# Optimization experiments

Measured on AMD Instinct MI355X. Metric: run time of the kernel, lower is better.

## Reference

```python
import jax, jax.numpy as jnp
import numpy as np

# Model hyperparameters (from init_kwargs)
CHANNEL_COUNT = 32   # C: features per element
MIXTURE_COUNT = 4    # K: number of class distributions
MIXTURE_SIZE = 4     # S: gaussian components per class
EM_ITERS = 3         # fixed EM refinement iterations
LOG2PI = 1.8378770664093453
COV_REG = 1e-4       # covariance diagonal regularizer
EPS = 1e-6


def setup_inputs() -> dict:
    key = jax.random.key(0)
    kf, kl = jax.random.split(key)
    features = jax.random.normal(kf, (4, CHANNEL_COUNT, 65536), dtype=jnp.float32)
    initial_labels = jax.random.randint(kl, (4, 65536), 0, MIXTURE_COUNT, dtype=jnp.int32)
    return {"features": features, "initial_labels": initial_labels}


def reference(features, initial_labels):
    # features: [B, C, N] float; initial_labels: [B, N] int in [0, K)
    B, C, N = features.shape
    K, S = MIXTURE_COUNT, MIXTURE_SIZE
    dt = features.dtype

    # class membership mask [B, K, N]
    mask = jax.nn.one_hot(initial_labels, K, dtype=dt).transpose(0, 2, 1)
    # deterministic initial within-class component assignment: element n -> component n % S
    comp_onehot = jax.nn.one_hot(jnp.arange(N) % S, S, dtype=dt).T  # [S, N]
    r = mask[:, :, None, :] * comp_onehot[None, None]               # [B, K, S, N]

    eye = COV_REG * jnp.eye(C, dtype=dt)
    logp = None
    for _ in range(EM_ITERS):
        # ---- M-step: per-component weight, mean, covariance (sufficient stats) ----
        w = r.sum(-1)                                                # [B, K, S]
        mu = jnp.einsum('bksn,bcn->bksc', r, features) / (w[..., None] + EPS)
        sxx = jnp.einsum('bksn,bcn,bdn->bkscd', r, features, features) / (w[..., None, None] + EPS)
        cov = sxx - jnp.einsum('bksc,bksd->bkscd', mu, mu) + eye     # [B, K, S, C, C]
        prec = jnp.linalg.inv(cov)
        _, logdet = jnp.linalg.slogdet(cov)                          # [B, K, S]
        pi = (w + EPS) / (w.sum(-1, keepdims=True) + S * EPS)        # mixing weights

        # ---- E-step: full-covariance gaussian log-density per element ----
        t = jnp.einsum('bkscd,bdn->bkscn', prec, features)           # [B, K, S, C, N]
        quad = (jnp.einsum('bcn,bkscn->bksn', features, t)
                - 2.0 * jnp.einsum('bksc,bkscn->bksn', mu, t)
                + jnp.einsum('bksc,bkscd,bksd->bks', mu, prec, mu)[..., None])
        logp = jnp.log(pi)[..., None] - 0.5 * (C * LOG2PI + logdet[..., None] + quad)  # [B,K,S,N]
        # responsibilities within each class, restricted to that class's labeled elements
        r = jax.nn.softmax(logp, axis=2) * mask[:, :, None, :]

    # per-class mixture log-likelihood for EVERY element, then posterior over classes
    class_ll = jax.nn.logsumexp(logp, axis=2)        # [B, K, N]
    output_logits = jax.nn.softmax(class_ll, axis=1)  # class assignment probabilities
    return output_logits
```

## Files before the change

### kernel.cpp

```cpp
#include <hip/hip_runtime.h>
#include <hip/hip_fp16.h>
#include <math.h>

#define BB 4
#define CC 32
#define KK 4
#define SS 4
#define NN 65536

constexpr int NCOMP = 64;
constexpr int SSTRIDE = 1088;
constexpr int PSTRIDE = 1128;
constexpr int NB = 128;
constexpr float EPS_ = 1e-6f;
constexpr float COVREG_ = 1e-4f;
constexpr float LOG2PI_C = 1.8378770664093453f;

__device__ constexpr int XOFF_[32] = {
    0,   4,   8,   12,  16,  24,  32,  40,  48,  60,  72,
    84,  96,  112, 128, 144, 160, 180, 200, 220, 240, 264,
    288, 312, 336, 364, 392, 420, 448, 480, 512, 544};

typedef _Float16 half8 __attribute__((ext_vector_type(8)));
typedef float floatx4 __attribute__((ext_vector_type(4)));

template <bool ITER0>
__global__ __launch_bounds__(256, 2) void gmm_accum_mfma(
    const float* __restrict__ feat, const int* __restrict__ labels,
    const float* __restrict__ resp, float* __restrict__ partials) {
  __shared__ __align__(16) float fC[32 * 36];
  __shared__ __align__(16) _Float16 respH[4][32];
  __shared__ __align__(16) _Float16 maskH[4][32];

  const int t = threadIdx.x;
  const int b = blockIdx.y;
  const int blk0 = blockIdx.x * 512;
  const int k = t >> 6;
  const int l = t & 63;
  const int row16 = l & 15;
  const int kg = l >> 4;

  floatx4 acc[4][7];
#pragma unroll
  for (int s = 0; s < 4; ++s)
#pragma unroll
    for (int j = 0; j < 7; ++j) acc[s][j] = (floatx4){0.f, 0.f, 0.f, 0.f};

  const int cstage = t >> 3;
  const int n4 = (t & 7) * 4;

  float4 pf;
  float4 presp = make_float4(0, 0, 0, 0);
  int plab = 0;
  pf = *(const float4*)(feat + ((size_t)b * CC + cstage) * NN + blk0 + n4);
  if (t < 32) {
    plab = labels[b * NN + blk0 + t];
    if (!ITER0) presp = *(const float4*)(resp + ((size_t)b * NN + blk0 + t) * 4);
  }

  const half8 hz = {0, 0, 0, 0, 0, 0, 0, 0};

  for (int chunk = 0; chunk < 16; ++chunk) {
    *(float4*)&fC[cstage * 36 + n4] = pf;
    if (t < 32) {
      if (ITER0) {
        const int cmp = (blk0 + chunk * 32 + t) & 3;
        respH[0][t] = (cmp == 0) ? (_Float16)1 : (_Float16)0;
        respH[1][t] = (cmp == 1) ? (_Float16)1 : (_Float16)0;
        respH[2][t] = (cmp == 2) ? (_Float16)1 : (_Float16)0;
        respH[3][t] = (cmp == 3) ? (_Float16)1 : (_Float16)0;
      } else {
        respH[0][t] = (_Float16)presp.x;
        respH[1][t] = (_Float16)presp.y;
        respH[2][t] = (_Float16)presp.z;
        respH[3][t] = (_Float16)presp.w;
      }
      maskH[0][t] = (plab == 0) ? (_Float16)1 : (_Float16)0;
      maskH[1][t] = (plab == 1) ? (_Float16)1 : (_Float16)0;
      maskH[2][t] = (plab == 2) ? (_Float16)1 : (_Float16)0;
      maskH[3][t] = (plab == 3) ? (_Float16)1 : (_Float16)0;
    }
    __syncthreads();

    if (chunk < 15) {
      const int n0n = blk0 + (chunk + 1) * 32;
      pf = *(const float4*)(feat + ((size_t)b * CC + cstage) * NN + n0n + n4);
      if (t < 32) {
        plab = labels[b * NN + n0n + t];
        if (!ITER0)
          presp = *(const float4*)(resp + ((size_t)b * NN + n0n + t) * 4);
      }
    }

    const float4 fa0 = *(const float4*)&fC[row16 * 36 + kg * 8];
    const float4 fa1 = *(const float4*)&fC[row16 * 36 + kg * 8 + 4];
    const float4 fb0 = *(const float4*)&fC[(row16 + 16) * 36 + kg * 8];
    const float4 fb1 = *(const float4*)&fC[(row16 + 16) * 36 + kg * 8 + 4];
    half8 ff0, ff1;
    ff0[0] = (_Float16)fa0.x; ff0[1] = (_Float16)fa0.y;
    ff0[2] = (_Float16)fa0.z; ff0[3] = (_Float16)fa0.w;
    ff0[4] = (_Float16)fa1.x; ff0[5] = (_Float16)fa1.y;
    ff0[6] = (_Float16)fa1.z; ff0[7] = (_Float16)fa1.w;
    ff1[0] = (_Float16)fb0.x; ff1[1] = (_Float16)fb0.y;
    ff1[2] = (_Float16)fb0.z; ff1[3] = (_Float16)fb0.w;
    ff1[4] = (_Float16)fb1.x; ff1[5] = (_Float16)fb1.y;
    ff1[6] = (_Float16)fb1.z; ff1[7] = (_Float16)fb1.w;

    const half8 mh = *(const half8*)&maskH[k][kg * 8];
    const half8 H0 = ff0 * mh;
    const half8 H1 = ff1 * mh;
    const half8 agB = (row16 == 0) ? mh : hz;

#pragma unroll
    for (int s = 0; s < 4; ++s) {
      const half8 rh = *(const half8*)&respH[s][kg * 8];
      const half8 G0 = ff0 * rh;
      const half8 G1 = ff1 * rh;
      const half8 agA = (row16 == 0) ? rh : hz;
      acc[s][0] =
          __builtin_amdgcn_mfma_f32_16x16x32_f16(G0, H0, acc[s][0], 0, 0, 0);
      acc[s][1] =
          __builtin_amdgcn_mfma_f32_16x16x32_f16(G0, H1, acc[s][1], 0, 0, 0);
      acc[s][2] =
          __builtin_amdgcn_mfma_f32_16x16x32_f16(G1, H0, acc[s][2], 0, 0, 0);
      acc[s][3] =
          __builtin_amdgcn_mfma_f32_16x16x32_f16(G1, H1, acc[s][3], 0, 0, 0);
      acc[s][4] =
          __builtin_amdgcn_mfma_f32_16x16x32_f16(G0, agB, acc[s][4], 0, 0, 0);
      acc[s][5] =
          __builtin_amdgcn_mfma_f32_16x16x32_f16(G1, agB, acc[s][5], 0, 0, 0);
      acc[s][6] =
          __builtin_amdgcn_mfma_f32_16x16x32_f16(agA, agB, acc[s][6], 0, 0, 0);
    }
    __syncthreads();
  }

#pragma unroll
  for (int s = 0; s < 4; ++s) {
    float* sg = partials +
                ((size_t)(b * NB + blockIdx.x) * 16 + (k * 4 + s)) * SSTRIDE;
    const int dr = kg * 4;
#pragma unroll
    for (int r = 0; r < 4; ++r) {
      sg[(dr + r) * 32 + row16] = acc[s][0][r];
      sg[(dr + r) * 32 + 16 + row16] = acc[s][1][r];
      sg[(16 + dr + r) * 32 + row16] = acc[s][2][r];
      sg[(16 + dr + r) * 32 + 16 + row16] = acc[s][3][r];
    }
    if (row16 == 0) {
#pragma unroll
      for (int r = 0; r < 4; ++r) {
        sg[1024 + dr + r] = acc[s][4][r];
        sg[1024 + 16 + dr + r] = acc[s][5][r];
      }
    }
    if (l == 0) sg[1056] = acc[s][6][0];
  }
}

template <bool ITER0, bool ATOMIC, int TILES>
__global__ __launch_bounds__(256, 1) void gmm_accum(
    const float* __restrict__ feat, const int* __restrict__ labels,
    const float* __restrict__ resp, float* __restrict__ outbuf) {
  __shared__ float fT[64 * 36];
  __shared__ float resp_lds[64 * 4];
  __shared__ int lab_lds[64];

  const int t = threadIdx.x;
  const int b = blockIdx.y;
  const int blk0 = blockIdx.x * (TILES * 64);

  const int wv = t >> 6;
  const int l = t & 63;
  const int sc = (t >> 4) & 3;
  const int p = t & 15;
  const int a0 = (p >> 2) * 8;
  const int b0 = (p & 3) * 8;

  float acc[8][8];
#pragma unroll
  for (int x = 0; x < 8; ++x)
#pragma unroll
    for (int y = 0; y < 8; ++y) acc[x][y] = 0.f;
  float sx[8] = {0, 0, 0, 0, 0, 0, 0, 0};
  float wacc = 0.f;

  const int cload = t >> 4;
  const int i4 = (t & 15) * 4;

  float4 pf0, pf1;
  float4 presp = make_float4(0, 0, 0, 0);
  int plab = 0;
  {
    const int n0 = blk0;
    pf0 = *(const float4*)(feat + ((size_t)b * CC + cload) * NN + n0 + i4);
    pf1 = *(const float4*)(feat + ((size_t)b * CC + cload + 16) * NN + n0 + i4);
    if (t < 64) {
      plab = labels[b * NN + n0 + t];
      if (!ITER0)
        presp = *(const float4*)(resp + ((size_t)b * NN + n0 + t) * 4);
    }
  }

  for (int tile = 0; tile < TILES; ++tile) {
    fT[(i4 + 0) * 36 + cload] = pf0.x;
    fT[(i4 + 1) * 36 + cload] = pf0.y;
    fT[(i4 + 2) * 36 + cload] = pf0.z;
    fT[(i4 + 3) * 36 + cload] = pf0.w;
    fT[(i4 + 0) * 36 + cload + 16] = pf1.x;
    fT[(i4 + 1) * 36 + cload + 16] = pf1.y;
    fT[(i4 + 2) * 36 + cload + 16] = pf1.z;
    fT[(i4 + 3) * 36 + cload + 16] = pf1.w;
    if (t < 64) {
      lab_lds[t] = plab;
      if (ITER0) {
        const int cmp = (blk0 + tile * 64 + t) & 3;
        resp_lds[t * 4 + 0] = (cmp == 0) ? 1.f : 0.f;
        resp_lds[t * 4 + 1] = (cmp == 1) ? 1.f : 0.f;
        resp_lds[t * 4 + 2] = (cmp == 2) ? 1.f : 0.f;
        resp_lds[t * 4 + 3] = (cmp == 3) ? 1.f : 0.f;
      } else {
        resp_lds[t * 4 + 0] = presp.x;
        resp_lds[t * 4 + 1] = presp.y;
        resp_lds[t * 4 + 2] = presp.z;
        resp_lds[t * 4 + 3] = presp.w;
      }
    }
    __syncthreads();
    if (tile < TILES - 1) {
      const int n0 = blk0 + (tile + 1) * 64;
      pf0 = *(const float4*)(feat + ((size_t)b * CC + cload) * NN + n0 + i4);
      pf1 =
          *(const float4*)(feat + ((size_t)b * CC + cload + 16) * NN + n0 + i4);
      if (t < 64) {
        plab = labels[b * NN + n0 + t];
        if (!ITER0)
          presp = *(const float4*)(resp + ((size_t)b * NN + n0 + t) * 4);
      }
    }

    unsigned long long m = __ballot(lab_lds[l] == wv);
    while (m) {
      const int i = __builtin_ctzll(m);
      m &= m - 1;
      const float rs = resp_lds[i * 4 + sc];
      const float4 ra0 = *(const float4*)&fT[i * 36 + a0];
      const float4 ra1 = *(const float4*)&fT[i * 36 + a0 + 4];
      const float4 rb0 = *(const float4*)&fT[i * 36 + b0];
      const float4 rb1 = *(const float4*)&fT[i * 36 + b0 + 4];
      const float ra[8] = {ra0.x, ra0.y, ra0.z, ra0.w,
                           ra1.x, ra1.y, ra1.z, ra1.w};
      const float rb[8] = {rb0.x, rb0.y, rb0.z, rb0.w,
                           rb1.x, rb1.y, rb1.z, rb1.w};
#pragma unroll
      for (int x = 0; x < 8; ++x) {
        const float v = rs * ra[x];
#pragma unroll
        for (int y = 0; y < 8; ++y) acc[x][y] = fmaf(v, rb[y], acc[x][y]);
      }
#pragma unroll
      for (int y = 0; y < 8; ++y) sx[y] = fmaf(rs, rb[y], sx[y]);
      wacc += rs;
    }
    __syncthreads();
  }

  if (ATOMIC) {
    float* sg = outbuf + ((size_t)(b * KK + wv) * SS + sc) * SSTRIDE;
#pragma unroll
    for (int x = 0; x < 8; ++x)
#pragma unroll
      for (int y = 0; y < 8; ++y)
        atomicAdd(sg + (a0 + x) * 32 + b0 + y, acc[x][y]);
    if (p < 4) {
#pragma unroll
      for (int y = 0; y < 8; ++y) atomicAdd(sg + 1024 + b0 + y, sx[y]);
    }
    if (p == 0) atomicAdd(sg + 1056, wacc);
  } else {
    const int nb = NN / (TILES * 64);
    float* sg = outbuf + ((size_t)(b * nb + blockIdx.x) * 16 + (wv * 4 + sc)) *
                             SSTRIDE;
#pragma unroll
    for (int x = 0; x < 8; ++x)
#pragma unroll
      for (int y = 0; y < 8; ++y) sg[(a0 + x) * 32 + b0 + y] = acc[x][y];
    if (p < 4) {
#pragma unroll
      for (int y = 0; y < 8; ++y) sg[1024 + b0 + y] = sx[y];
    }
    if (p == 0) sg[1056] = wacc;
  }
}

__global__ __launch_bounds__(256) void gmm_reduce(const float* __restrict__ part,
                                                  float* __restrict__ stats,
                                                  int nb) {
  const int idx = blockIdx.x * 256 + threadIdx.x;
  if (idx >= NCOMP * 1057) return;
  const int comp = idx / 1057;
  const int cell = idx - comp * 1057;
  const int b = comp >> 4, cl = comp & 15;
  const float* src = part + ((size_t)(b * nb) * 16 + cl) * SSTRIDE + cell;
  const size_t stride = (size_t)16 * SSTRIDE;
  float s0 = 0.f, s1 = 0.f;
#pragma unroll 8
  for (int blk = 0; blk < nb; blk += 2) {
    s0 += src[(size_t)blk * stride];
    s1 += src[(size_t)(blk + 1) * stride];
  }
  stats[(size_t)comp * SSTRIDE + cell] = s0 + s1;
}

__global__ __launch_bounds__(64) void gmm_params(const float* __restrict__ stats,
                                                 float* __restrict__ params) {
  __shared__ float Xl[32 * 33];
  __shared__ float mul[32];

  const int t = threadIdx.x;
  const int i = t & 31;
  const int comp = blockIdx.x;
  const float* sg = stats + (size_t)comp * SSTRIDE;

  const float w = sg[1056];
  const float invw = 1.f / (w + EPS_);
  const float mu_i = sg[1024 + i] * invw;

  float a[32];
#pragma unroll
  for (int j4 = 0; j4 < 8; ++j4) {
    const float4 v = *(const float4*)(sg + i * 32 + 4 * j4);
    a[4 * j4 + 0] = v.x;
    a[4 * j4 + 1] = v.y;
    a[4 * j4 + 2] = v.z;
    a[4 * j4 + 3] = v.w;
  }
#pragma unroll
  for (int j = 0; j < 32; ++j) {
    const float muj = sg[1024 + j] * invw;
    float v = fmaf(a[j], invw, -mu_i * muj);
    v = (j == i) ? v + COVREG_ : v;
    a[j] = v;
  }

  float ldet = 0.f;
  float rd[32];
#pragma unroll
  for (int j = 0; j < 32; ++j) {
    const float diag = __shfl(a[j], j);
    ldet += logf(diag);
    const float rinv = rsqrtf(diag);
    rd[j] = rinv;
    const float lij = a[j] * rinv;
    a[j] = (i >= j) ? lij : a[j];
#pragma unroll
    for (int m = j + 1; m < 32; ++m) {
      const float Lmj = __shfl(lij, m);
      a[m] = (i >= m) ? fmaf(-lij, Lmj, a[m]) : a[m];
    }
  }

  float x[32];
#pragma unroll
  for (int m = 0; m < 32; ++m) {
    float s = (m == i) ? 1.f : 0.f;
#pragma unroll
    for (int r = 0; r < m; ++r) {
      const float Lmr = __shfl(a[r], m);
      s = fmaf(-Lmr, x[r], s);
    }
    x[m] = s * rd[m];
  }

  if (t < 32) {
#pragma unroll
    for (int m = 0; m < 32; ++m) Xl[m * 33 + i] = x[m];
    mul[i] = mu_i;
  }
  __syncthreads();

  float* pg = params + (size_t)comp * PSTRIDE;
  for (int r = 0; r < 32; ++r) {
    const int L4 = 4 * ((r >> 2) + 1);
    if (t < L4) pg[XOFF_[r] + t] = (t <= r) ? Xl[r * 33 + t] : 0.f;
  }
  {
    __half* xh = (__half*)(pg + 612);
#pragma unroll
    for (int th = 0; th < 2; ++th) {
      const int row = th * 16 + (t & 15);
      const int k0 = (t >> 4) * 8;
#pragma unroll
      for (int j = 0; j < 8; ++j) {
        const int k = k0 + j;
        const float v = (k <= row) ? Xl[row * 33 + k] : 0.f;
        xh[(th * 64 + t) * 8 + j] = __float2half(v);
      }
    }
  }
  if (t < 32) {
    float z = 0.f;
    for (int j = 0; j <= t; ++j) z += Xl[t * 33 + j] * mul[j];
    pg[576 + t] = z;
  }
  if (t == 0) {
    const int sib = comp & ~3;
    float wsum = 0.f;
    for (int s2 = 0; s2 < 4; ++s2)
      wsum += stats[(size_t)(sib + s2) * SSTRIDE + 1056];
    const float pi = (w + EPS_) / (wsum + SS * EPS_);
    pg[608] = logf(pi) - 0.5f * (CC * LOG2PI_C + ldet);
  }
}

template <int TILES>
__global__ __launch_bounds__(256, 2) void gmm_estep_own4(
    const float* __restrict__ feat, const int* __restrict__ labels,
    const float* __restrict__ params, float* __restrict__ resp) {
  __shared__ float fT[64 * 36];
  __shared__ int4 xlds4[2048];
  __shared__ float zlds[16 * 32];
  __shared__ float c0lds[16];
  __shared__ int lab_lds[64];

  const int t = threadIdx.x;
  const int b = blockIdx.y;
  const int blk0 = blockIdx.x * (TILES * 64);
  const int w = t >> 6;
  const int l = t & 63;
  const int row16 = l & 15;
  const int kg = l >> 4;

  for (int idx = t; idx < 2048; idx += 256) {
    const int c = idx >> 7, chunk = idx & 127;
    xlds4[idx] = *(const int4*)((const char*)(params +
                                              (size_t)(b * 16 + c) * PSTRIDE +
                                              612) +
                                chunk * 16);
  }
  for (int idx = t; idx < 16 * 32; idx += 256) {
    zlds[idx] =
        params[(size_t)(b * 16 + (idx >> 5)) * PSTRIDE + 576 + (idx & 31)];
  }
  if (t < 16) c0lds[t] = params[(size_t)(b * 16 + t) * PSTRIDE + 608];

  const _Float16* xl = (const _Float16*)xlds4;
  const int cload = t >> 4;
  const int i4 = (t & 15) * 4;
  const floatx4 zero4 = {0.f, 0.f, 0.f, 0.f};

  for (int tile = 0; tile < TILES; ++tile) {
    const int base = blk0 + tile * 64;
    {
      const float4 v0 =
          *(const float4*)(feat + ((size_t)b * CC + cload) * NN + base + i4);
      const float4 v1 = *(const float4*)(feat +
                                         ((size_t)b * CC + cload + 16) * NN +
                                         base + i4);
      fT[(i4 + 0) * 36 + cload] = v0.x;
      fT[(i4 + 1) * 36 + cload] = v0.y;
      fT[(i4 + 2) * 36 + cload] = v0.z;
      fT[(i4 + 3) * 36 + cload] = v0.w;
      fT[(i4 + 0) * 36 + cload + 16] = v1.x;
      fT[(i4 + 1) * 36 + cload + 16] = v1.y;
      fT[(i4 + 2) * 36 + cload + 16] = v1.z;
      fT[(i4 + 3) * 36 + cload + 16] = v1.w;
      if (t < 64) lab_lds[t] = labels[b * NN + base + t];
    }
    __syncthreads();

    const int eoff = (w * 16 + row16) * 36 + kg * 8;
    const float4 fv0 = *(const float4*)&fT[eoff];
    const float4 fv1 = *(const float4*)&fT[eoff + 4];
    half8 bfr;
    bfr[0] = (_Float16)fv0.x;
    bfr[1] = (_Float16)fv0.y;
    bfr[2] = (_Float16)fv0.z;
    bfr[3] = (_Float16)fv0.w;
    bfr[4] = (_Float16)fv1.x;
    bfr[5] = (_Float16)fv1.y;
    bfr[6] = (_Float16)fv1.z;
    bfr[7] = (_Float16)fv1.w;

    const int lab = lab_lds[w * 16 + row16];

    float lp0 = 0.f, lp1 = 0.f, lp2 = 0.f, lp3 = 0.f;
#pragma unroll
    for (int c = 0; c < 16; ++c) {
      const half8 a0 = *(const half8*)&xl[c * 1024 + (0 * 64 + l) * 8];
      const half8 a1 = *(const half8*)&xl[c * 1024 + (1 * 64 + l) * 8];
      floatx4 y0 =
          __builtin_amdgcn_mfma_f32_16x16x32_f16(a0, bfr, zero4, 0, 0, 0);
      floatx4 y1 =
          __builtin_amdgcn_mfma_f32_16x16x32_f16(a1, bfr, zero4, 0, 0, 0);
      const float4 zv0 = *(const float4*)&zlds[c * 32 + kg * 4];
      const float4 zv1 = *(const float4*)&zlds[c * 32 + 16 + kg * 4];
      float q = 0.f;
      {
        const float d0 = y0[0] - zv0.x;
        const float d1 = y0[1] - zv0.y;
        const float d2 = y0[2] - zv0.z;
        const float d3 = y0[3] - zv0.w;
        q = fmaf(d0, d0, q);
        q = fmaf(d1, d1, q);
        q = fmaf(d2, d2, q);
        q = fmaf(d3, d3, q);
        const float e0 = y1[0] - zv1.x;
        const float e1 = y1[1] - zv1.y;
        const float e2 = y1[2] - zv1.z;
        const float e3 = y1[3] - zv1.w;
        q = fmaf(e0, e0, q);
        q = fmaf(e1, e1, q);
        q = fmaf(e2, e2, q);
        q = fmaf(e3, e3, q);
      }
      q += __shfl_xor(q, 16);
      q += __shfl_xor(q, 32);
      const float lp = c0lds[c] - 0.5f * q;
      const bool own = (c >> 2) == lab;
      const int s = c & 3;
      lp0 = (own && s == 0) ? lp : lp0;
      lp1 = (own && s == 1) ? lp : lp1;
      lp2 = (own && s == 2) ? lp : lp2;
      lp3 = (own && s == 3) ? lp : lp3;
    }

    const float m = fmaxf(fmaxf(lp0, lp1), fmaxf(lp2, lp3));
    const float e0 = expf(lp0 - m), e1 = expf(lp1 - m);
    const float e2 = expf(lp2 - m), e3 = expf(lp3 - m);
    const float inv = 1.f / (e0 + e1 + e2 + e3);
    if (l < 16) {
      *(float4*)(resp + ((size_t)b * NN + base + w * 16 + l) * 4) =
          make_float4(e0 * inv, e1 * inv, e2 * inv, e3 * inv);
    }
    __syncthreads();
  }
}

template <int TILES>
__global__ __launch_bounds__(256, 2) void gmm_estep_final4(
    const float* __restrict__ feat, const float* __restrict__ params,
    float* __restrict__ out) {
  __shared__ float fT[64 * 36];
  __shared__ int4 xlds4[2048];
  __shared__ float zlds[16 * 32];
  __shared__ float c0lds[16];

  const int t = threadIdx.x;
  const int b = blockIdx.y;
  const int blk0 = blockIdx.x * (TILES * 64);
  const int w = t >> 6;
  const int l = t & 63;
  const int row16 = l & 15;
  const int kg = l >> 4;

  for (int idx = t; idx < 2048; idx += 256) {
    const int c = idx >> 7, chunk = idx & 127;
    xlds4[idx] = *(const int4*)((const char*)(params +
                                              (size_t)(b * 16 + c) * PSTRIDE +
                                              612) +
                                chunk * 16);
  }
  for (int idx = t; idx < 16 * 32; idx += 256) {
    zlds[idx] =
        params[(size_t)(b * 16 + (idx >> 5)) * PSTRIDE + 576 + (idx & 31)];
  }
  if (t < 16) c0lds[t] = params[(size_t)(b * 16 + t) * PSTRIDE + 608];

  const _Float16* xl = (const _Float16*)xlds4;
  const int cload = t >> 4;
  const int i4 = (t & 15) * 4;
  const floatx4 zero4 = {0.f, 0.f, 0.f, 0.f};

  for (int tile = 0; tile < TILES; ++tile) {
    const int base = blk0 + tile * 64;
    {
      const float4 v0 =
          *(const float4*)(feat + ((size_t)b * CC + cload) * NN + base + i4);
      const float4 v1 = *(const float4*)(feat +
                                         ((size_t)b * CC + cload + 16) * NN +
                                         base + i4);
      fT[(i4 + 0) * 36 + cload] = v0.x;
      fT[(i4 + 1) * 36 + cload] = v0.y;
      fT[(i4 + 2) * 36 + cload] = v0.z;
      fT[(i4 + 3) * 36 + cload] = v0.w;
      fT[(i4 + 0) * 36 + cload + 16] = v1.x;
      fT[(i4 + 1) * 36 + cload + 16] = v1.y;
      fT[(i4 + 2) * 36 + cload + 16] = v1.z;
      fT[(i4 + 3) * 36 + cload + 16] = v1.w;
    }
    __syncthreads();

    const int eoff = (w * 16 + row16) * 36 + kg * 8;
    const float4 fv0 = *(const float4*)&fT[eoff];
    const float4 fv1 = *(const float4*)&fT[eoff + 4];
    half8 bfr;
    bfr[0] = (_Float16)fv0.x;
    bfr[1] = (_Float16)fv0.y;
    bfr[2] = (_Float16)fv0.z;
    bfr[3] = (_Float16)fv0.w;
    bfr[4] = (_Float16)fv1.x;
    bfr[5] = (_Float16)fv1.y;
    bfr[6] = (_Float16)fv1.z;
    bfr[7] = (_Float16)fv1.w;

    float lp[16];
#pragma unroll
    for (int c = 0; c < 16; ++c) {
      const half8 a0 = *(const half8*)&xl[c * 1024 + (0 * 64 + l) * 8];
      const half8 a1 = *(const half8*)&xl[c * 1024 + (1 * 64 + l) * 8];
      floatx4 y0 =
          __builtin_amdgcn_mfma_f32_16x16x32_f16(a0, bfr, zero4, 0, 0, 0);
      floatx4 y1 =
          __builtin_amdgcn_mfma_f32_16x16x32_f16(a1, bfr, zero4, 0, 0, 0);
      const float4 zv0 = *(const float4*)&zlds[c * 32 + kg * 4];
      const float4 zv1 = *(const float4*)&zlds[c * 32 + 16 + kg * 4];
      float q = 0.f;
      {
        const float d0 = y0[0] - zv0.x;
        const float d1 = y0[1] - zv0.y;
        const float d2 = y0[2] - zv0.z;
        const float d3 = y0[3] - zv0.w;
        q = fmaf(d0, d0, q);
        q = fmaf(d1, d1, q);
        q = fmaf(d2, d2, q);
        q = fmaf(d3, d3, q);
        const float e0 = y1[0] - zv1.x;
        const float e1 = y1[1] - zv1.y;
        const float e2 = y1[2] - zv1.z;
        const float e3 = y1[3] - zv1.w;
        q = fmaf(e0, e0, q);
        q = fmaf(e1, e1, q);
        q = fmaf(e2, e2, q);
        q = fmaf(e3, e3, q);
      }
      q += __shfl_xor(q, 16);
      q += __shfl_xor(q, 32);
      lp[c] = c0lds[c] - 0.5f * q;
    }

    float cll[4];
#pragma unroll
    for (int k = 0; k < 4; ++k) {
      const float m = fmaxf(fmaxf(lp[4 * k + 0], lp[4 * k + 1]),
                            fmaxf(lp[4 * k + 2], lp[4 * k + 3]));
      const float s = expf(lp[4 * k + 0] - m) + expf(lp[4 * k + 1] - m) +
                      expf(lp[4 * k + 2] - m) + expf(lp[4 * k + 3] - m);
      cll[k] = m + logf(s);
    }
    const float m = fmaxf(fmaxf(cll[0], cll[1]), fmaxf(cll[2], cll[3]));
    const float e0 = expf(cll[0] - m), e1 = expf(cll[1] - m);
    const float e2 = expf(cll[2] - m), e3 = expf(cll[3] - m);
    const float inv = 1.f / (e0 + e1 + e2 + e3);
    if (l < 16) {
      const int n = base + w * 16 + l;
      out[((size_t)b * KK + 0) * NN + n] = e0 * inv;
      out[((size_t)b * KK + 1) * NN + n] = e1 * inv;
      out[((size_t)b * KK + 2) * NN + n] = e2 * inv;
      out[((size_t)b * KK + 3) * NN + n] = e3 * inv;
    }
    __syncthreads();
  }
}

extern "C" void kernel_launch(void* const* d_in, const int* in_sizes, int n_in,
                              void* d_out, int out_size, void* d_ws,
                              size_t ws_size, hipStream_t stream) {
  const float* feat = (const float*)d_in[0];
  const int* labels = (const int*)d_in[1];
  float* out = (float*)d_out;

  float* stats = (float*)d_ws;
  float* params = stats + (size_t)NCOMP * SSTRIDE;
  float* resp_ws = params + (size_t)NCOMP * PSTRIDE;
  float* partials = resp_ws + (size_t)BB * NN * 4;

  const size_t resp_end_b =
      ((size_t)NCOMP * SSTRIDE + (size_t)NCOMP * PSTRIDE + (size_t)BB * NN * 4) *
      sizeof(float);
  const size_t part_end_b =
      resp_end_b + (size_t)BB * NB * 16 * SSTRIDE * sizeof(float);
  const bool have_resp = ws_size >= resp_end_b;
  const bool have_part = ws_size >= part_end_b;
  float* resp = have_resp ? resp_ws : out;

  const int reduce_blocks = (NCOMP * 1057 + 255) / 256;

  for (int it = 0; it < 3; ++it) {
    if (have_part) {
      if (it == 0)
        gmm_accum_mfma<true>
            <<<dim3(NB, BB), 256, 0, stream>>>(feat, labels, resp, partials);
      else
        gmm_accum_mfma<false>
            <<<dim3(NB, BB), 256, 0, stream>>>(feat, labels, resp, partials);
      gmm_reduce<<<reduce_blocks, 256, 0, stream>>>(partials, stats, NB);
    } else {
      hipMemsetAsync(stats, 0, (size_t)NCOMP * SSTRIDE * sizeof(float), stream);
      if (it == 0)
        gmm_accum<true, true, 16>
            <<<dim3(64, BB), 256, 0, stream>>>(feat, labels, resp, stats);
      else
        gmm_accum<false, true, 16>
            <<<dim3(64, BB), 256, 0, stream>>>(feat, labels, resp, stats);
    }
    gmm_params<<<NCOMP, 64, 0, stream>>>(stats, params);
    if (it < 2)
      gmm_estep_own4<8><<<dim3(NN / 512, BB), 256, 0, stream>>>(feat, labels,
                                                                params, resp);
    else
      gmm_estep_final4<8><<<dim3(NN / 512, BB), 256, 0, stream>>>(feat, params,
                                                                  out);
  }
}
```

Measured before the change: 276.6 us.

## Fuse E-step responsibilities with next M-step MFMA accumulation into one kernel

Adds a gmm_fused kernel that computes each tile's own-class responsibilities and immediately accumulates the weighted sufficient statistics (second moments, means, weights) with fp16 MFMA, writing per-block partials. Iterations 1 and 2 no longer write the responsibilities buffer to global memory and read it back, and the features are read once per iteration instead of twice. The cost is that responsibilities and masked features are rounded to fp16 before accumulation, and the fused kernel holds more accumulator registers and LDS.

```diff
diff --git a/kernel.cpp b/kernel.cpp
--- a/kernel.cpp
+++ b/kernel.cpp
@@ -158,270 +158,18 @@
   }
 }
 
-template <bool ITER0, bool ATOMIC, int TILES>
-__global__ __launch_bounds__(256, 1) void gmm_accum(
+template <int TILES>
+__global__ __launch_bounds__(256, 2) void gmm_fused(
     const float* __restrict__ feat, const int* __restrict__ labels,
-    const float* __restrict__ resp, float* __restrict__ outbuf) {
+    const float* __restrict__ params, float* __restrict__ partials) {
   __shared__ float fT[64 * 36];
-  __shared__ float resp_lds[64 * 4];
-  __shared__ int lab_lds[64];
-
-  const int t = threadIdx.x;
-  const int b = blockIdx.y;
-  const int blk0 = blockIdx.x * (TILES * 64);
-
-  const int wv = t >> 6;
-  const int l = t & 63;
-  const int sc = (t >> 4) & 3;
-  const int p = t & 15;
-  const int a0 = (p >> 2) * 8;
-  const int b0 = (p & 3) * 8;
-
-  float acc[8][8];
-#pragma unroll
-  for (int x = 0; x < 8; ++x)
-#pragma unroll
-    for (int y = 0; y < 8; ++y) acc[x][y] = 0.f;
-  float sx[8] = {0, 0, 0, 0, 0, 0, 0, 0};
-  float wacc = 0.f;
-
-  const int cload = t >> 4;
-  const int i4 = (t & 15) * 4;
-
-  float4 pf0, pf1;
-  float4 presp = make_float4(0, 0, 0, 0);
-  int plab = 0;
-  {
-    const int n0 = blk0;
-    pf0 = *(const float4*)(feat + ((size_t)b * CC + cload) * NN + n0 + i4);
-    pf1 = *(const float4*)(feat + ((size_t)b * CC + cload + 16) * NN + n0 + i4);
-    if (t < 64) {
-      plab = labels[b * NN + n0 + t];
-      if (!ITER0)
-        presp = *(const float4*)(resp + ((size_t)b * NN + n0 + t) * 4);
-    }
-  }
-
-  for (int tile = 0; tile < TILES; ++tile) {
-    fT[(i4 + 0) * 36 + cload] = pf0.x;
-    fT[(i4 + 1) * 36 + cload] = pf0.y;
-    fT[(i4 + 2) * 36 + cload] = pf0.z;
-    fT[(i4 + 3) * 36 + cload] = pf0.w;
-    fT[(i4 + 0) * 36 + cload + 16] = pf1.x;
-    fT[(i4 + 1) * 36 + cload + 16] = pf1.y;
-    fT[(i4 + 2) * 36 + cload + 16] = pf1.z;
-    fT[(i4 + 3) * 36 + cload + 16] = pf1.w;
-    if (t < 64) {
-      lab_lds[t] = plab;
-      if (ITER0) {
-        const int cmp = (blk0 + tile * 64 + t) & 3;
-        resp_lds[t * 4 + 0] = (cmp == 0) ? 1.f : 0.f;
-        resp_lds[t * 4 + 1] = (cmp == 1) ? 1.f : 0.f;
-        resp_lds[t * 4 + 2] = (cmp == 2) ? 1.f : 0.f;
-        resp_lds[t * 4 + 3] = (cmp == 3) ? 1.f : 0.f;
-      } else {
-        resp_lds[t * 4 + 0] = presp.x;
-        resp_lds[t * 4 + 1] = presp.y;
-        resp_lds[t * 4 + 2] = presp.z;
-        resp_lds[t * 4 + 3] = presp.w;
-      }
-    }
-    __syncthreads();
-    if (tile < TILES - 1) {
-      const int n0 = blk0 + (tile + 1) * 64;
-      pf0 = *(const float4*)(feat + ((size_t)b * CC + cload) * NN + n0 + i4);
-      pf1 =
-          *(const float4*)(feat + ((size_t)b * CC + cload + 16) * NN + n0 + i4);
-      if (t < 64) {
-        plab = labels[b * NN + n0 + t];
-        if (!ITER0)
-          presp = *(const float4*)(resp + ((size_t)b * NN + n0 + t) * 4);
-      }
-    }
-
-    unsigned long long m = __ballot(lab_lds[l] == wv);
-    while (m) {
-      const int i = __builtin_ctzll(m);
-      m &= m - 1;
-      const float rs = resp_lds[i * 4 + sc];
-      const float4 ra0 = *(const float4*)&fT[i * 36 + a0];
-      const float4 ra1 = *(const float4*)&fT[i * 36 + a0 + 4];
-      const float4 rb0 = *(const float4*)&fT[i * 36 + b0];
-      const float4 rb1 = *(const float4*)&fT[i * 36 + b0 + 4];
-      const float ra[8] = {ra0.x, ra0.y, ra0.z, ra0.w,
-                           ra1.x, ra1.y, ra1.z, ra1.w};
-      const float rb[8] = {rb0.x, rb0.y, rb0.z, rb0.w,
-                           rb1.x, rb1.y, rb1.z, rb1.w};
-#pragma unroll
-      for (int x = 0; x < 8; ++x) {
-        const float v = rs * ra[x];
-#pragma unroll
-        for (int y = 0; y < 8; ++y) acc[x][y] = fmaf(v, rb[y], acc[x][y]);
-      }
-#pragma unroll
-      for (int y = 0; y < 8; ++y) sx[y] = fmaf(rs, rb[y], sx[y]);
-      wacc += rs;
-    }
-    __syncthreads();
-  }
-
-  if (ATOMIC) {
-    float* sg = outbuf + ((size_t)(b * KK + wv) * SS + sc) * SSTRIDE;
-#pragma unroll
-    for (int x = 0; x < 8; ++x)
-#pragma unroll
-      for (int y = 0; y < 8; ++y)
-        atomicAdd(sg + (a0 + x) * 32 + b0 + y, acc[x][y]);
-    if (p < 4) {
-#pragma unroll
-      for (int y = 0; y < 8; ++y) atomicAdd(sg + 1024 + b0 + y, sx[y]);
-    }
-    if (p == 0) atomicAdd(sg + 1056, wacc);
-  } else {
-    const int nb = NN / (TILES * 64);
-    float* sg = outbuf + ((size_t)(b * nb + blockIdx.x) * 16 + (wv * 4 + sc)) *
-                             SSTRIDE;
-#pragma unroll
-    for (int x = 0; x < 8; ++x)
-#pragma unroll
-      for (int y = 0; y < 8; ++y) sg[(a0 + x) * 32 + b0 + y] = acc[x][y];
-    if (p < 4) {
-#pragma unroll
-      for (int y = 0; y < 8; ++y) sg[1024 + b0 + y] = sx[y];
-    }
-    if (p == 0) sg[1056] = wacc;
-  }
-}
-
-__global__ __launch_bounds__(256) void gmm_reduce(const float* __restrict__ part,
-                                                  float* __restrict__ stats,
-                                                  int nb) {
-  const int idx = blockIdx.x * 256 + threadIdx.x;
-  if (idx >= NCOMP * 1057) return;
-  const int comp = idx / 1057;
-  const int cell = idx - comp * 1057;
-  const int b = comp >> 4, cl = comp & 15;
-  const float* src = part + ((size_t)(b * nb) * 16 + cl) * SSTRIDE + cell;
-  const size_t stride = (size_t)16 * SSTRIDE;
-  float s0 = 0.f, s1 = 0.f;
-#pragma unroll 8
-  for (int blk = 0; blk < nb; blk += 2) {
-    s0 += src[(size_t)blk * stride];
-    s1 += src[(size_t)(blk + 1) * stride];
-  }
-  stats[(size_t)comp * SSTRIDE + cell] = s0 + s1;
-}
-
-__global__ __launch_bounds__(64) void gmm_params(const float* __restrict__ stats,
-                                                 float* __restrict__ params) {
-  __shared__ float Xl[32 * 33];
-  __shared__ float mul[32];
-
-  const int t = threadIdx.x;
-  const int i = t & 31;
-  const int comp = blockIdx.x;
-  const float* sg = stats + (size_t)comp * SSTRIDE;
-
-  const float w = sg[1056];
-  const float invw = 1.f / (w + EPS_);
-  const float mu_i = sg[1024 + i] * invw;
-
-  float a[32];
-#pragma unroll
-  for (int j4 = 0; j4 < 8; ++j4) {
-    const float4 v = *(const float4*)(sg + i * 32 + 4 * j4);
-    a[4 * j4 + 0] = v.x;
-    a[4 * j4 + 1] = v.y;
-    a[4 * j4 + 2] = v.z;
-    a[4 * j4 + 3] = v.w;
-  }
-#pragma unroll
-  for (int j = 0; j < 32; ++j) {
-    const float muj = sg[1024 + j] * invw;
-    float v = fmaf(a[j], invw, -mu_i * muj);
-    v = (j == i) ? v + COVREG_ : v;
-    a[j] = v;
-  }
-
-  float ldet = 0.f;
-  float rd[32];
-#pragma unroll
-  for (int j = 0; j < 32; ++j) {
-    const float diag = __shfl(a[j], j);
-    ldet += logf(diag);
-    const float rinv = rsqrtf(diag);
-    rd[j] = rinv;
-    const float lij = a[j] * rinv;
-    a[j] = (i >= j) ? lij : a[j];
-#pragma unroll
-    for (int m = j + 1; m < 32; ++m) {
-      const float Lmj = __shfl(lij, m);
-      a[m] = (i >= m) ? fmaf(-lij, Lmj, a[m]) : a[m];
-    }
-  }
-
-  float x[32];
-#pragma unroll
-  for (int m = 0; m < 32; ++m) {
-    float s = (m == i) ? 1.f : 0.f;
-#pragma unroll
-    for (int r = 0; r < m; ++r) {
-      const float Lmr = __shfl(a[r], m);
-      s = fmaf(-Lmr, x[r], s);
-    }
-    x[m] = s * rd[m];
-  }
-
-  if (t < 32) {
-#pragma unroll
-    for (int m = 0; m < 32; ++m) Xl[m * 33 + i] = x[m];
-    mul[i] = mu_i;
-  }
-  __syncthreads();
-
-  float* pg = params + (size_t)comp * PSTRIDE;
-  for (int r = 0; r < 32; ++r) {
-    const int L4 = 4 * ((r >> 2) + 1);
-    if (t < L4) pg[XOFF_[r] + t] = (t <= r) ? Xl[r * 33 + t] : 0.f;
-  }
-  {
-    __half* xh = (__half*)(pg + 612);
-#pragma unroll
-    for (int th = 0; th < 2; ++th) {
-      const int row = th * 16 + (t & 15);
-      const int k0 = (t >> 4) * 8;
-#pragma unroll
-      for (int j = 0; j < 8; ++j) {
-        const int k = k0 + j;
-        const float v = (k <= row) ? Xl[row * 33 + k] : 0.f;
-        xh[(th * 64 + t) * 8 + j] = __float2half(v);
-      }
-    }
-  }
-  if (t < 32) {
-    float z = 0.f;
-    for (int j = 0; j <= t; ++j) z += Xl[t * 33 + j] * mul[j];
-    pg[576 + t] = z;
-  }
-  if (t == 0) {
-    const int sib = comp & ~3;
-    float wsum = 0.f;
-    for (int s2 = 0; s2 < 4; ++s2)
-      wsum += stats[(size_t)(sib + s2) * SSTRIDE + 1056];
-    const float pi = (w + EPS_) / (wsum + SS * EPS_);
-    pg[608] = logf(pi) - 0.5f * (CC * LOG2PI_C + ldet);
-  }
-}
-
-template <int TILES>
-__global__ __launch_bounds__(256, 2) void gmm_estep_own4(
-    const float* __restrict__ feat, const int* __restrict__ labels,
-    const float* __restrict__ params, float* __restrict__ resp) {
-  __shared__ float fT[64 * 36];
+  __shared__ __align__(16) float fC[32 * 68];
   __shared__ int4 xlds4[2048];
   __shared__ float zlds[16 * 32];
   __shared__ float c0lds[16];
   __shared__ int lab_lds[64];
+  __shared__ __align__(16) _Float16 respH[4][64];
+  __shared__ __align__(16) _Float16 maskH[4][64];
 
   const int t = threadIdx.x;
   const int b = blockIdx.y;
@@ -448,6 +196,13 @@
   const int cload = t >> 4;
   const int i4 = (t & 15) * 4;
   const floatx4 zero4 = {0.f, 0.f, 0.f, 0.f};
+  const half8 hz = {0, 0, 0, 0, 0, 0, 0, 0};
+
+  floatx4 acc[4][7];
+#pragma unroll
+  for (int s = 0; s < 4; ++s)
+#pragma unroll
+    for (int j = 0; j < 7; ++j) acc[s][j] = (floatx4){0.f, 0.f, 0.f, 0.f};
 
   for (int tile = 0; tile < TILES; ++tile) {
     const int base = blk0 + tile * 64;
@@ -465,6 +220,8 @@
       fT[(i4 + 1) * 36 + cload + 16] = v1.y;
       fT[(i4 + 2) * 36 + cload + 16] = v1.z;
       fT[(i4 + 3) * 36 + cload + 16] = v1.w;
+      *(float4*)&fC[cload * 68 + i4] = v0;
+      *(float4*)&fC[(cload + 16) * 68 + i4] = v1;
       if (t < 64) lab_lds[t] = labels[b * NN + base + t];
     }
     __syncthreads();
@@ -525,26 +282,363 @@
       lp3 = (own && s == 3) ? lp : lp3;
     }
 
-    const float m = fmaxf(fmaxf(lp0, lp1), fmaxf(lp2, lp3));
-    const float e0 = expf(lp0 - m), e1 = expf(lp1 - m);
-    const float e2 = expf(lp2 - m), e3 = expf(lp3 - m);
-    const float inv = 1.f / (e0 + e1 + e2 + e3);
-    if (l < 16) {
-      *(float4*)(resp + ((size_t)b * NN + base + w * 16 + l) * 4) =
-          make_float4(e0 * inv, e1 * inv, e2 * inv, e3 * inv);
-    }
-    __syncthreads();
+    {
+      const float m = fmaxf(fmaxf(lp0, lp1), fmaxf(lp2, lp3));
+      const float e0 = expf(lp0 - m), e1 = expf(lp1 - m);
+      const float e2 = expf(lp2 - m), e3 = expf(lp3 - m);
+      const float inv = 1.f / (e0 + e1 + e2 + e3);
+      if (l < 16) {
+        const int e = w * 16 + l;
+        respH[0][e] = (_Float16)(e0 * inv);
+        respH[1][e] = (_Float16)(e1 * inv);
+        respH[2][e] = (_Float16)(e2 * inv);
+        respH[3][e] = (_Float16)(e3 * inv);
+      }
+      if (t < 64) {
+        const int lb2 = lab_lds[t];
+        maskH[0][t] = (lb2 == 0) ? (_Float16)1 : (_Float16)0;
+        maskH[1][t] = (lb2 == 1) ? (_Float16)1 : (_Float16)0;
+        maskH[2][t] = (lb2 == 2) ? (_Float16)1 : (_Float16)0;
+        maskH[3][t] = (lb2 == 3) ? (_Float16)1 : (_Float16)0;
+      }
+    }
+    __syncthreads();
+
+#pragma unroll
+    for (int h = 0; h < 2; ++h) {
+      const int eb = h * 32;
+      const float4 fa0 = *(const float4*)&fC[row16 * 68 + eb + kg * 8];
+      const float4 fa1 = *(const float4*)&fC[row16 * 68 + eb + kg * 8 + 4];
+      const float4 fb0 = *(const float4*)&fC[(row16 + 16) * 68 + eb + kg * 8];
+      const float4 fb1 =
+          *(const float4*)&fC[(row16 + 16) * 68 + eb + kg * 8 + 4];
+      half8 ff0, ff1;
+      ff0[0] = (_Float16)fa0.x; ff0[1] = (_Float16)fa0.y;
+      ff0[2] = (_Float16)fa0.z; ff0[3] = (_Float16)fa0.w;
+      ff0[4] = (_Float16)fa1.x; ff0[5] = (_Float16)fa1.y;
+      ff0[6] = (_Float16)fa1.z; ff0[7] = (_Float16)fa1.w;
+      ff1[0] = (_Float16)fb0.x; ff1[1] = (_Float16)fb0.y;
+      ff1[2] = (_Float16)fb0.z; ff1[3] = (_Float16)fb0.w;
+      ff1[4] = (_Float16)fb1.x; ff1[5] = (_Float16)fb1.y;
+      ff1[6] = (_Float16)fb1.z; ff1[7] = (_Float16)fb1.w;
+
+      const half8 mh = *(const half8*)&maskH[w][eb + kg * 8];
+      const half8 H0 = ff0 * mh;
+      const half8 H1 = ff1 * mh;
+      const half8 agB = (row16 == 0) ? mh : hz;
+
+#pragma unroll
+      for (int s = 0; s < 4; ++s) {
+        const half8 rh = *(const half8*)&respH[s][eb + kg * 8];
+        const half8 G0 = ff0 * rh;
+        const half8 G1 = ff1 * rh;
+        const half8 agA = (row16 == 0) ? rh : hz;
+        acc[s][0] =
+            __builtin_amdgcn_mfma_f32_16x16x32_f16(G0, H0, acc[s][0], 0, 0, 0);
+        acc[s][1] =
+            __builtin_amdgcn_mfma_f32_16x16x32_f16(G0, H1, acc[s][1], 0, 0, 0);
+        acc[s][2] =
+            __builtin_amdgcn_mfma_f32_16x16x32_f16(G1, H0, acc[s][2], 0, 0, 0);
+        acc[s][3] =
+            __builtin_amdgcn_mfma_f32_16x16x32_f16(G1, H1, acc[s][3], 0, 0, 0);
+        acc[s][4] =
+            __builtin_amdgcn_mfma_f32_16x16x32_f16(G0, agB, acc[s][4], 0, 0, 0);
+        acc[s][5] =
+            __builtin_amdgcn_mfma_f32_16x16x32_f16(G1, agB, acc[s][5], 0, 0, 0);
+        acc[s][6] = __builtin_amdgcn_mfma_f32_16x16x32_f16(agA, agB, acc[s][6],
+                                                           0, 0, 0);
+      }
+    }
+    __syncthreads();
+  }
+
+#pragma unroll
+  for (int s = 0; s < 4; ++s) {
+    float* sg = partials +
+                ((size_t)(b * NB + blockIdx.x) * 16 + (w * 4 + s)) * SSTRIDE;
+    const int dr = kg * 4;
+#pragma unroll
+    for (int r = 0; r < 4; ++r) {
+      sg[(dr + r) * 32 + row16] = acc[s][0][r];
+      sg[(dr + r) * 32 + 16 + row16] = acc[s][1][r];
+      sg[(16 + dr + r) * 32 + row16] = acc[s][2][r];
+      sg[(16 + dr + r) * 32 + 16 + row16] = acc[s][3][r];
+    }
+    if (row16 == 0) {
+#pragma unroll
+      for (int r = 0; r < 4; ++r) {
+        sg[1024 + dr + r] = acc[s][4][r];
+        sg[1024 + 16 + dr + r] = acc[s][5][r];
+      }
+    }
+    if (l == 0) sg[1056] = acc[s][6][0];
   }
 }
 
+template <bool ITER0, bool ATOMIC, int TILES>
+__global__ __launch_bounds__(256, 1) void gmm_accum(
+    const float* __restrict__ feat, const int* __restrict__ labels,
+    const float* __restrict__ resp, float* __restrict__ outbuf) {
+  __shared__ float fT[64 * 36];
+  __shared__ float resp_lds[64 * 4];
+  __shared__ int lab_lds[64];
+
+  const int t = threadIdx.x;
+  const int b = blockIdx.y;
+  const int blk0 = blockIdx.x * (TILES * 64);
+
+  const int wv = t >> 6;
+  const int l = t & 63;
+  const int sc = (t >> 4) & 3;
+  const int p = t & 15;
+  const int a0 = (p >> 2) * 8;
+  const int b0 = (p & 3) * 8;
+
+  float acc[8][8];
+#pragma unroll
+  for (int x = 0; x < 8; ++x)
+#pragma unroll
+    for (int y = 0; y < 8; ++y) acc[x][y] = 0.f;
+  float sx[8] = {0, 0, 0, 0, 0, 0, 0, 0};
+  float wacc = 0.f;
+
+  const int cload = t >> 4;
+  const int i4 = (t & 15) * 4;
+
+  float4 pf0, pf1;
+  float4 presp = make_float4(0, 0, 0, 0);
+  int plab = 0;
+  {
+    const int n0 = blk0;
+    pf0 = *(const float4*)(feat + ((size_t)b * CC + cload) * NN + n0 + i4);
+    pf1 = *(const float4*)(feat + ((size_t)b * CC + cload + 16) * NN + n0 + i4);
+    if (t < 64) {
+      plab = labels[b * NN + n0 + t];
+      if (!ITER0)
+        presp = *(const float4*)(resp + ((size_t)b * NN + n0 + t) * 4);
+    }
+  }
+
+  for (int tile = 0; tile < TILES; ++tile) {
+    fT[(i4 + 0) * 36 + cload] = pf0.x;
+    fT[(i4 + 1) * 36 + cload] = pf0.y;
+    fT[(i4 + 2) * 36 + cload] = pf0.z;
+    fT[(i4 + 3) * 36 + cload] = pf0.w;
+    fT[(i4 + 0) * 36 + cload + 16] = pf1.x;
+    fT[(i4 + 1) * 36 + cload + 16] = pf1.y;
+    fT[(i4 + 2) * 36 + cload + 16] = pf1.z;
+    fT[(i4 + 3) * 36 + cload + 16] = pf1.w;
+    if (t < 64) {
+      lab_lds[t] = plab;
+      if (ITER0) {
+        const int cmp = (blk0 + tile * 64 + t) & 3;
+        resp_lds[t * 4 + 0] = (cmp == 0) ? 1.f : 0.f;
+        resp_lds[t * 4 + 1] = (cmp == 1) ? 1.f : 0.f;
+        resp_lds[t * 4 + 2] = (cmp == 2) ? 1.f : 0.f;
+        resp_lds[t * 4 + 3] = (cmp == 3) ? 1.f : 0.f;
+      } else {
+        resp_lds[t * 4 + 0] = presp.x;
+        resp_lds[t * 4 + 1] = presp.y;
+        resp_lds[t * 4 + 2] = presp.z;
+        resp_lds[t * 4 + 3] = presp.w;
+      }
+    }
+    __syncthreads();
+    if (tile < TILES - 1) {
+      const int n0 = blk0 + (tile + 1) * 64;
+      pf0 = *(const float4*)(feat + ((size_t)b * CC + cload) * NN + n0 + i4);
+      pf1 =
+          *(const float4*)(feat + ((size_t)b * CC + cload + 16) * NN + n0 + i4);
+      if (t < 64) {
+        plab = labels[b * NN + n0 + t];
+        if (!ITER0)
+          presp = *(const float4*)(resp + ((size_t)b * NN + n0 + t) * 4);
+      }
+    }
+
+    unsigned long long m = __ballot(lab_lds[l] == wv);
+    while (m) {
+      const int i = __builtin_ctzll(m);
+      m &= m - 1;
+      const float rs = resp_lds[i * 4 + sc];
+      const float4 ra0 = *(const float4*)&fT[i * 36 + a0];
+      const float4 ra1 = *(const float4*)&fT[i * 36 + a0 + 4];
+      const float4 rb0 = *(const float4*)&fT[i * 36 + b0];
+      const float4 rb1 = *(const float4*)&fT[i * 36 + b0 + 4];
+      const float ra[8] = {ra0.x, ra0.y, ra0.z, ra0.w,
+                           ra1.x, ra1.y, ra1.z, ra1.w};
+      const float rb[8] = {rb0.x, rb0.y, rb0.z, rb0.w,
+                           rb1.x, rb1.y, rb1.z, rb1.w};
+#pragma unroll
+      for (int x = 0; x < 8; ++x) {
+        const float v = rs * ra[x];
+#pragma unroll
+        for (int y = 0; y < 8; ++y) acc[x][y] = fmaf(v, rb[y], acc[x][y]);
+      }
+#pragma unroll
+      for (int y = 0; y < 8; ++y) sx[y] = fmaf(rs, rb[y], sx[y]);
+      wacc += rs;
+    }
+    __syncthreads();
+  }
+
+  if (ATOMIC) {
+    float* sg = outbuf + ((size_t)(b * KK + wv) * SS + sc) * SSTRIDE;
+#pragma unroll
+    for (int x = 0; x < 8; ++x)
+#pragma unroll
+      for (int y = 0; y < 8; ++y)
+        atomicAdd(sg + (a0 + x) * 32 + b0 + y, acc[x][y]);
+    if (p < 4) {
+#pragma unroll
+      for (int y = 0; y < 8; ++y) atomicAdd(sg + 1024 + b0 + y, sx[y]);
+    }
+    if (p == 0) atomicAdd(sg + 1056, wacc);
+  } else {
+    const int nb = NN / (TILES * 64);
+    float* sg = outbuf + ((size_t)(b * nb + blockIdx.x) * 16 + (wv * 4 + sc)) *
+                             SSTRIDE;
+#pragma unroll
+    for (int x = 0; x < 8; ++x)
+#pragma unroll
+      for (int y = 0; y < 8; ++y) sg[(a0 + x) * 32 + b0 + y] = acc[x][y];
+    if (p < 4) {
+#pragma unroll
+      for (int y = 0; y < 8; ++y) sg[1024 + b0 + y] = sx[y];
+    }
+    if (p == 0) sg[1056] = wacc;
+  }
+}
+
+__global__ __launch_bounds__(256) void gmm_reduce(const float* __restrict__ part,
+                                                  float* __restrict__ stats,
+                                                  int nb) {
+  const int idx = blockIdx.x * 256 + threadIdx.x;
+  if (idx >= NCOMP * 1057) return;
+  const int comp = idx / 1057;
+  const int cell = idx - comp * 1057;
+  const int b = comp >> 4, cl = comp & 15;
+  const float* src = part + ((size_t)(b * nb) * 16 + cl) * SSTRIDE + cell;
+  const size_t stride = (size_t)16 * SSTRIDE;
+  float s0 = 0.f, s1 = 0.f;
+#pragma unroll 8
+  for (int blk = 0; blk < nb; blk += 2) {
+    s0 += src[(size_t)blk * stride];
+    s1 += src[(size_t)(blk + 1) * stride];
+  }
+  stats[(size_t)comp * SSTRIDE + cell] = s0 + s1;
+}
+
+__global__ __launch_bounds__(64) void gmm_params(const float* __restrict__ stats,
+                                                 float* __restrict__ params) {
+  __shared__ float Xl[32 * 33];
+  __shared__ float mul[32];
+
+  const int t = threadIdx.x;
+  const int i = t & 31;
+  const int comp = blockIdx.x;
+  const float* sg = stats + (size_t)comp * SSTRIDE;
+
+  const float w = sg[1056];
+  const float invw = 1.f / (w + EPS_);
+  const float mu_i = sg[1024 + i] * invw;
+
+  float a[32];
+#pragma unroll
+  for (int j4 = 0; j4 < 8; ++j4) {
+    const float4 v = *(const float4*)(sg + i * 32 + 4 * j4);
+    a[4 * j4 + 0] = v.x;
+    a[4 * j4 + 1] = v.y;
+    a[4 * j4 + 2] = v.z;
+    a[4 * j4 + 3] = v.w;
+  }
+#pragma unroll
+  for (int j = 0; j < 32; ++j) {
+    const float muj = sg[1024 + j] * invw;
+    float v = fmaf(a[j], invw, -mu_i * muj);
+    v = (j == i) ? v + COVREG_ : v;
+    a[j] = v;
+  }
+
+  float ldet = 0.f;
+  float rd[32];
+#pragma unroll
+  for (int j = 0; j < 32; ++j) {
+    const float diag = __shfl(a[j], j);
+    ldet += logf(diag);
+    const float rinv = rsqrtf(diag);
+    rd[j] = rinv;
+    const float lij = a[j] * rinv;
+    a[j] = (i >= j) ? lij : a[j];
+#pragma unroll
+    for (int m = j + 1; m < 32; ++m) {
+      const float Lmj = __shfl(lij, m);
+      a[m] = (i >= m) ? fmaf(-lij, Lmj, a[m]) : a[m];
+    }
+  }
+
+  float x[32];
+#pragma unroll
+  for (int m = 0; m < 32; ++m) {
+    float s = (m == i) ? 1.f : 0.f;
+#pragma unroll
+    for (int r = 0; r < m; ++r) {
+      const float Lmr = __shfl(a[r], m);
+      s = fmaf(-Lmr, x[r], s);
+    }
+    x[m] = s * rd[m];
+  }
+
+  if (t < 32) {
+#pragma unroll
+    for (int m = 0; m < 32; ++m) Xl[m * 33 + i] = x[m];
+    mul[i] = mu_i;
+  }
+  __syncthreads();
+
+  float* pg = params + (size_t)comp * PSTRIDE;
+  for (int r = 0; r < 32; ++r) {
+    const int L4 = 4 * ((r >> 2) + 1);
+    if (t < L4) pg[XOFF_[r] + t] = (t <= r) ? Xl[r * 33 + t] : 0.f;
+  }
+  {
+    __half* xh = (__half*)(pg + 612);
+#pragma unroll
+    for (int th = 0; th < 2; ++th) {
+      const int row = th * 16 + (t & 15);
+      const int k0 = (t >> 4) * 8;
+#pragma unroll
+      for (int j = 0; j < 8; ++j) {
+        const int k = k0 + j;
+        const float v = (k <= row) ? Xl[row * 33 + k] : 0.f;
+        xh[(th * 64 + t) * 8 + j] = __float2half(v);
+      }
+    }
+  }
+  if (t < 32) {
+    float z = 0.f;
+    for (int j = 0; j <= t; ++j) z += Xl[t * 33 + j] * mul[j];
+    pg[576 + t] = z;
+  }
+  if (t == 0) {
+    const int sib = comp & ~3;
+    float wsum = 0.f;
+    for (int s2 = 0; s2 < 4; ++s2)
+      wsum += stats[(size_t)(sib + s2) * SSTRIDE + 1056];
+    const float pi = (w + EPS_) / (wsum + SS * EPS_);
+    pg[608] = logf(pi) - 0.5f * (CC * LOG2PI_C + ldet);
+  }
+}
+
 template <int TILES>
-__global__ __launch_bounds__(256, 2) void gmm_estep_final4(
-    const float* __restrict__ feat, const float* __restrict__ params,
-    float* __restrict__ out) {
+__global__ __launch_bounds__(256, 2) void gmm_estep_own4(
+    const float* __restrict__ feat, const int* __restrict__ labels,
+    const float* __restrict__ params, float* __restrict__ resp) {
   __shared__ float fT[64 * 36];
   __shared__ int4 xlds4[2048];
   __shared__ float zlds[16 * 32];
   __shared__ float c0lds[16];
+  __shared__ int lab_lds[64];
 
   const int t = threadIdx.x;
   const int b = blockIdx.y;
@@ -588,6 +682,7 @@
       fT[(i4 + 1) * 36 + cload + 16] = v1.y;
       fT[(i4 + 2) * 36 + cload + 16] = v1.z;
       fT[(i4 + 3) * 36 + cload + 16] = v1.w;
+      if (t < 64) lab_lds[t] = labels[b * NN + base + t];
     }
     __syncthreads();
 
@@ -604,7 +699,9 @@
     bfr[6] = (_Float16)fv1.z;
     bfr[7] = (_Float16)fv1.w;
 
-    float lp[16];
+    const int lab = lab_lds[w * 16 + row16];
+
+    float lp0 = 0.f, lp1 = 0.f, lp2 = 0.f, lp3 = 0.f;
 #pragma unroll
     for (int c = 0; c < 16; ++c) {
       const half8 a0 = *(const half8*)&xl[c * 1024 + (0 * 64 + l) * 8];
@@ -636,6 +733,126 @@
       }
       q += __shfl_xor(q, 16);
       q += __shfl_xor(q, 32);
+      const float lp = c0lds[c] - 0.5f * q;
+      const bool own = (c >> 2) == lab;
+      const int s = c & 3;
+      lp0 = (own && s == 0) ? lp : lp0;
+      lp1 = (own && s == 1) ? lp : lp1;
+      lp2 = (own && s == 2) ? lp : lp2;
+      lp3 = (own && s == 3) ? lp : lp3;
+    }
+
+    const float m = fmaxf(fmaxf(lp0, lp1), fmaxf(lp2, lp3));
+    const float e0 = expf(lp0 - m), e1 = expf(lp1 - m);
+    const float e2 = expf(lp2 - m), e3 = expf(lp3 - m);
+    const float inv = 1.f / (e0 + e1 + e2 + e3);
+    if (l < 16) {
+      *(float4*)(resp + ((size_t)b * NN + base + w * 16 + l) * 4) =
+          make_float4(e0 * inv, e1 * inv, e2 * inv, e3 * inv);
+    }
+    __syncthreads();
+  }
+}
+
+template <int TILES>
+__global__ __launch_bounds__(256, 2) void gmm_estep_final4(
+    const float* __restrict__ feat, const float* __restrict__ params,
+    float* __restrict__ out) {
+  __shared__ float fT[64 * 36];
+  __shared__ int4 xlds4[2048];
+  __shared__ float zlds[16 * 32];
+  __shared__ float c0lds[16];
+
+  const int t = threadIdx.x;
+  const int b = blockIdx.y;
+  const int blk0 = blockIdx.x * (TILES * 64);
+  const int w = t >> 6;
+  const int l = t & 63;
+  const int row16 = l & 15;
+  const int kg = l >> 4;
+
+  for (int idx = t; idx < 2048; idx += 256) {
+    const int c = idx >> 7, chunk = idx & 127;
+    xlds4[idx] = *(const int4*)((const char*)(params +
+                                              (size_t)(b * 16 + c) * PSTRIDE +
+                                              612) +
+                                chunk * 16);
+  }
+  for (int idx = t; idx < 16 * 32; idx += 256) {
+    zlds[idx] =
+        params[(size_t)(b * 16 + (idx >> 5)) * PSTRIDE + 576 + (idx & 31)];
+  }
+  if (t < 16) c0lds[t] = params[(size_t)(b * 16 + t) * PSTRIDE + 608];
+
+  const _Float16* xl = (const _Float16*)xlds4;
+  const int cload = t >> 4;
+  const int i4 = (t & 15) * 4;
+  const floatx4 zero4 = {0.f, 0.f, 0.f, 0.f};
+
+  for (int tile = 0; tile < TILES; ++tile) {
+    const int base = blk0 + tile * 64;
+    {
+      const float4 v0 =
+          *(const float4*)(feat + ((size_t)b * CC + cload) * NN + base + i4);
+      const float4 v1 = *(const float4*)(feat +
+                                         ((size_t)b * CC + cload + 16) * NN +
+                                         base + i4);
+      fT[(i4 + 0) * 36 + cload] = v0.x;
+      fT[(i4 + 1) * 36 + cload] = v0.y;
+      fT[(i4 + 2) * 36 + cload] = v0.z;
+      fT[(i4 + 3) * 36 + cload] = v0.w;
+      fT[(i4 + 0) * 36 + cload + 16] = v1.x;
+      fT[(i4 + 1) * 36 + cload + 16] = v1.y;
+      fT[(i4 + 2) * 36 + cload + 16] = v1.z;
+      fT[(i4 + 3) * 36 + cload + 16] = v1.w;
+    }
+    __syncthreads();
+
+    const int eoff = (w * 16 + row16) * 36 + kg * 8;
+    const float4 fv0 = *(const float4*)&fT[eoff];
+    const float4 fv1 = *(const float4*)&fT[eoff + 4];
+    half8 bfr;
+    bfr[0] = (_Float16)fv0.x;
+    bfr[1] = (_Float16)fv0.y;
+    bfr[2] = (_Float16)fv0.z;
+    bfr[3] = (_Float16)fv0.w;
+    bfr[4] = (_Float16)fv1.x;
+    bfr[5] = (_Float16)fv1.y;
+    bfr[6] = (_Float16)fv1.z;
+    bfr[7] = (_Float16)fv1.w;
+
+    float lp[16];
+#pragma unroll
+    for (int c = 0; c < 16; ++c) {
+      const half8 a0 = *(const half8*)&xl[c * 1024 + (0 * 64 + l) * 8];
+      const half8 a1 = *(const half8*)&xl[c * 1024 + (1 * 64 + l) * 8];
+      floatx4 y0 =
+          __builtin_amdgcn_mfma_f32_16x16x32_f16(a0, bfr, zero4, 0, 0, 0);
+      floatx4 y1 =
+          __builtin_amdgcn_mfma_f32_16x16x32_f16(a1, bfr, zero4, 0, 0, 0);
+      const float4 zv0 = *(const float4*)&zlds[c * 32 + kg * 4];
+      const float4 zv1 = *(const float4*)&zlds[c * 32 + 16 + kg * 4];
+      float q = 0.f;
+      {
+        const float d0 = y0[0] - zv0.x;
+        const float d1 = y0[1] - zv0.y;
+        const float d2 = y0[2] - zv0.z;
+        const float d3 = y0[3] - zv0.w;
+        q = fmaf(d0, d0, q);
+        q = fmaf(d1, d1, q);
+        q = fmaf(d2, d2, q);
+        q = fmaf(d3, d3, q);
+        const float e0 = y1[0] - zv1.x;
+        const float e1 = y1[1] - zv1.y;
+        const float e2 = y1[2] - zv1.z;
+        const float e3 = y1[3] - zv1.w;
+        q = fmaf(e0, e0, q);
+        q = fmaf(e1, e1, q);
+        q = fmaf(e2, e2, q);
+        q = fmaf(e3, e3, q);
+      }
+      q += __shfl_xor(q, 16);
+      q += __shfl_xor(q, 32);
       lp[c] = c0lds[c] - 0.5f * q;
     }
 
@@ -686,16 +903,21 @@
 
   const int reduce_blocks = (NCOMP * 1057 + 255) / 256;
 
-  for (int it = 0; it < 3; ++it) {
-    if (have_part) {
-      if (it == 0)
-        gmm_accum_mfma<true>
-            <<<dim3(NB, BB), 256, 0, stream>>>(feat, labels, resp, partials);
-      else
-        gmm_accum_mfma<false>
-            <<<dim3(NB, BB), 256, 0, stream>>>(feat, labels, resp, partials);
+  if (have_part) {
+    gmm_accum_mfma<true>
+        <<<dim3(NB, BB), 256, 0, stream>>>(feat, labels, out, partials);
+    gmm_reduce<<<reduce_blocks, 256, 0, stream>>>(partials, stats, NB);
+    gmm_params<<<NCOMP, 64, 0, stream>>>(stats, params);
+    for (int it = 1; it < 3; ++it) {
+      gmm_fused<8>
+          <<<dim3(NB, BB), 256, 0, stream>>>(feat, labels, params, partials);
       gmm_reduce<<<reduce_blocks, 256, 0, stream>>>(partials, stats, NB);
-    } else {
+      gmm_params<<<NCOMP, 64, 0, stream>>>(stats, params);
+    }
+    gmm_estep_final4<8><<<dim3(NN / 512, BB), 256, 0, stream>>>(feat, params,
+                                                                out);
+  } else {
+    for (int it = 0; it < 3; ++it) {
       hipMemsetAsync(stats, 0, (size_t)NCOMP * SSTRIDE * sizeof(float), stream);
       if (it == 0)
         gmm_accum<true, true, 16>
@@ -703,13 +925,13 @@
       else
         gmm_accum<false, true, 16>
             <<<dim3(64, BB), 256, 0, stream>>>(feat, labels, resp, stats);
-    }
-    gmm_params<<<NCOMP, 64, 0, stream>>>(stats, params);
-    if (it < 2)
-      gmm_estep_own4<8><<<dim3(NN / 512, BB), 256, 0, stream>>>(feat, labels,
-                                                                params, resp);
-    else
-      gmm_estep_final4<8><<<dim3(NN / 512, BB), 256, 0, stream>>>(feat, params,
-                                                                  out);
+      gmm_params<<<NCOMP, 64, 0, stream>>>(stats, params);
+      if (it < 2)
+        gmm_estep_own4<8><<<dim3(NN / 512, BB), 256, 0, stream>>>(feat, labels,
+                                                                  params, resp);
+      else
+        gmm_estep_final4<8><<<dim3(NN / 512, BB), 256, 0, stream>>>(
+            feat, params, out);
+    }
   }
 }
```

New measurement: 278.0 us. Within noise of the previous version (+0.5%).
